# Performance work log

Hardware: AMD Instinct MI355X
Metric: run time of the kernel (lower is better)

Reference implementation:

```python
import jax, jax.numpy as jnp
import numpy as np
import math

B, S, HID = 2, 2048, 2048
NH, NKV, HD = 32, 8, 64
THETA = 10000.0
EPS = 1e-6
LAYER_IDX = 1
LAMBDA_INIT = 0.8 - 0.6 * math.exp(-0.3 * LAYER_IDX)
LAMBDA_STD = 0.1


def setup_inputs() -> dict:
    key = jax.random.key(0)
    ks = jax.random.split(key, 10)
    hidden_states = jax.random.normal(ks[0], (B, S, HID), jnp.float32)
    # RoPE cos/sin, llama convention: emb = cat(freqs, freqs)
    inv_freq = 1.0 / (THETA ** (np.arange(0, HD, 2, dtype=np.float32) / HD))
    freqs = np.outer(np.arange(S, dtype=np.float32), inv_freq)  # [S, HD/2]
    emb = np.concatenate([freqs, freqs], axis=-1)                # [S, HD]
    cos = jnp.broadcast_to(jnp.asarray(np.cos(emb), jnp.float32)[None], (B, S, HD))
    sin = jnp.broadcast_to(jnp.asarray(np.sin(emb), jnp.float32)[None], (B, S, HD))
    # additive causal mask [B,1,S,S]
    causal = jnp.triu(jnp.full((S, S), -1e9, dtype=jnp.float32), k=1)
    attention_mask = jnp.broadcast_to(causal[None, None], (B, 1, S, S))
    sc = 0.02
    wq = sc * jax.random.normal(ks[1], (NH * HD, HID), jnp.float32)
    wk = sc * jax.random.normal(ks[2], (NKV * HD, HID), jnp.float32)
    wv = sc * jax.random.normal(ks[3], (NKV * HD, HID), jnp.float32)
    wo = sc * jax.random.normal(ks[4], (HID, NH * HD), jnp.float32)
    lambda_q1 = LAMBDA_STD * jax.random.normal(ks[5], (HD,), jnp.float32)
    lambda_k1 = LAMBDA_STD * jax.random.normal(ks[6], (HD,), jnp.float32)
    lambda_q2 = LAMBDA_STD * jax.random.normal(ks[7], (HD,), jnp.float32)
    lambda_k2 = LAMBDA_STD * jax.random.normal(ks[8], (HD,), jnp.float32)
    return {"hidden_states": hidden_states, "cos": cos, "sin": sin,
            "attention_mask": attention_mask, "wq": wq, "wk": wk, "wv": wv,
            "wo": wo, "lambda_q1": lambda_q1, "lambda_k1": lambda_k1,
            "lambda_q2": lambda_q2, "lambda_k2": lambda_k2}


def _rotate_half(x):
    x1, x2 = jnp.split(x, 2, axis=-1)
    return jnp.concatenate([-x2, x1], axis=-1)


def reference(hidden_states, cos, sin, attention_mask, wq, wk, wv, wo,
              lambda_q1, lambda_k1, lambda_q2, lambda_k2):
    b, s, _ = hidden_states.shape
    # projections -> [b, h, s, d]
    q = jnp.einsum('bsh,oh->bso', hidden_states, wq).reshape(b, s, NH, HD).transpose(0, 2, 1, 3)
    k = jnp.einsum('bsh,oh->bso', hidden_states, wk).reshape(b, s, NKV, HD).transpose(0, 2, 1, 3)
    v = jnp.einsum('bsh,oh->bso', hidden_states, wv).reshape(b, s, NKV, HD).transpose(0, 2, 1, 3)
    # rotary
    c, sn = cos[:, None], sin[:, None]  # [b,1,s,d]
    q = q * c + _rotate_half(q) * sn
    k = k * c + _rotate_half(k) * sn
    # GQA repeat
    groups = NH // NKV
    k = jnp.repeat(k, groups, axis=1)
    v = jnp.repeat(v, groups, axis=1)
    # diff-attention value trick: pair head i with head i+NH/2 -> [b, NH, s, 2d]
    v = jnp.concatenate([v[:, :NH // 2], v[:, NH // 2:]], axis=-1)  # [b, NH/2, s, 2d]
    v = jnp.concatenate([v, v], axis=1)                              # [b, NH, s, 2d]
    # scores + causal mask, stable softmax in fp32
    aw = jnp.einsum('bhqd,bhkd->bhqk', q, k) / math.sqrt(HD)
    aw = aw + attention_mask
    aw = jax.nn.softmax(aw.astype(jnp.float32), axis=-1).astype(q.dtype)
    ao = jnp.einsum('bhqk,bhkd->bhqd', aw, v)  # [b, NH, s, 2d]
    lam1 = jnp.exp(jnp.sum((lambda_q1 * lambda_k1).astype(jnp.float32)))
    lam2 = jnp.exp(jnp.sum((lambda_q2 * lambda_k2).astype(jnp.float32)))
    lam = (lam1 - lam2).astype(q.dtype) + LAMBDA_INIT
    a1, a2 = ao[:, :NH // 2], ao[:, NH // 2:]
    out = a1 - lam * a2  # [b, NH/2, s, 2d]
    # RMSNorm over last dim (no affine)
    out = out * jax.lax.rsqrt(jnp.mean(out * out, axis=-1, keepdims=True) + EPS)
    out = (1.0 - LAMBDA_INIT) * out
    out = out.transpose(0, 2, 1, 3).reshape(b, s, NH * HD)
    return jnp.einsum('bso,ho->bsh', out, wo)
```

## Files before the change

### kernel.cpp

```cpp
#include <hip/hip_runtime.h>

typedef __attribute__((ext_vector_type(8))) short bhalf8;
typedef __attribute__((ext_vector_type(4))) float floatx4;

constexpr int B_ = 2, S_ = 2048, HID_ = 2048, NH_ = 32, NKV_ = 8, HD_ = 64;
constexpr float LAMBDA_INIT_F = 0.35550906759096924f;
constexpr float EPS_ = 1e-6f;
constexpr float QSCALE_ = 0.18033688011112042f;

#define DEVINL __device__ __forceinline__

DEVINL float bf2f(unsigned short u) {
    union { unsigned u; float f; } v; v.u = ((unsigned)u) << 16; return v.f;
}
DEVINL unsigned short f2bf(float f) {
    union { float f; unsigned u; } v; v.f = f;
    unsigned u = v.u;
    return (unsigned short)((u + 0x7fffu + ((u >> 16) & 1u)) >> 16);
}
DEVINL float fexp2(float x) {
#if __has_builtin(__builtin_amdgcn_exp2f)
    return __builtin_amdgcn_exp2f(x);
#else
    return exp2f(x);
#endif
}
DEVINL unsigned pk_bf16(float a, float b) {
#if __has_builtin(__builtin_amdgcn_cvt_pk_bf16_f32)
    typedef __bf16 bf16x2_t __attribute__((ext_vector_type(2)));
    bf16x2_t p = __builtin_amdgcn_cvt_pk_bf16_f32(a, b);
    unsigned r;
    __builtin_memcpy(&r, &p, 4);
    return r;
#else
    return (unsigned)f2bf(a) | ((unsigned)f2bf(b) << 16);
#endif
}
DEVINL void load_lds16(const unsigned short* g, unsigned short* l) {
    __builtin_amdgcn_global_load_lds(
        (const __attribute__((address_space(1))) unsigned int*)g,
        (__attribute__((address_space(3))) unsigned int*)l, 16, 0, 0);
}

__global__ void cvt_f32_bf16(const float* __restrict__ src, unsigned short* __restrict__ dst, int n) {
    int i = (blockIdx.x * 256 + threadIdx.x) * 4;
    if (i < n) {
        float4 v = *(const float4*)(src + i);
        ushort4 o;
        o.x = f2bf(v.x); o.y = f2bf(v.y); o.z = f2bf(v.z); o.w = f2bf(v.w);
        *(ushort4*)(dst + i) = o;
    }
}

__global__ void lam_kernel(const float* __restrict__ q1, const float* __restrict__ k1,
                           const float* __restrict__ q2, const float* __restrict__ k2,
                           float* __restrict__ lam) {
    const int l = threadIdx.x;
    float p1 = q1[l] * k1[l];
    float p2 = q2[l] * k2[l];
    #pragma unroll
    for (int off = 1; off < 64; off <<= 1) {
        p1 += __shfl_xor(p1, off, 64);
        p2 += __shfl_xor(p2, off, 64);
    }
    if (l == 0) *lam = expf(p1) - expf(p2) + LAMBDA_INIT_F;
}

template <bool OUT_BF16>
__global__ __launch_bounds__(256)
void gemm_bt(const unsigned short* __restrict__ A, const unsigned short* __restrict__ Bw,
             void* __restrict__ Cout, int M, int N, int K) {
    __shared__ __align__(16) unsigned short As[128][32];
    __shared__ __align__(16) unsigned short Bs[128][32];
    const int t = threadIdx.x;
    const int w = t >> 6, lane = t & 63, quad = lane >> 4, lid = lane & 15;
    const int wr = (w >> 1) * 64, wc = (w & 1) * 64;
    const long bm = (long)blockIdx.x * 128, bn = (long)blockIdx.y * 128;

    floatx4 acc[4][4];
    #pragma unroll
    for (int i = 0; i < 4; i++)
        #pragma unroll
        for (int j = 0; j < 4; j++) acc[i][j] = (floatx4){0.f, 0.f, 0.f, 0.f};

    const int s0 = t, s1 = t + 256;
    const unsigned short* Ag0 = A + (bm + (s0 >> 2)) * (long)K + (s0 & 3) * 8;
    const unsigned short* Ag1 = A + (bm + (s1 >> 2)) * (long)K + (s1 & 3) * 8;
    const unsigned short* Bg0 = Bw + (bn + (s0 >> 2)) * (long)K + (s0 & 3) * 8;
    const unsigned short* Bg1 = Bw + (bn + (s1 >> 2)) * (long)K + (s1 & 3) * 8;
    unsigned short* Al0 = &As[0][0] + s0 * 8;
    unsigned short* Al1 = &As[0][0] + s1 * 8;
    unsigned short* Bl0 = &Bs[0][0] + s0 * 8;
    unsigned short* Bl1 = &Bs[0][0] + s1 * 8;

    for (int kt = 0; kt < K; kt += 32) {
        __syncthreads();
        load_lds16(Ag0 + kt, Al0);
        load_lds16(Ag1 + kt, Al1);
        load_lds16(Bg0 + kt, Bl0);
        load_lds16(Bg1 + kt, Bl1);
        __syncthreads();
        bhalf8 af[4], bf[4];
        #pragma unroll
        for (int i = 0; i < 4; i++) af[i] = *(const bhalf8*)&As[wr + i * 16 + lid][quad * 8];
        #pragma unroll
        for (int j = 0; j < 4; j++) bf[j] = *(const bhalf8*)&Bs[wc + j * 16 + lid][quad * 8];
        #pragma unroll
        for (int i = 0; i < 4; i++)
            #pragma unroll
            for (int j = 0; j < 4; j++)
                acc[i][j] = __builtin_amdgcn_mfma_f32_16x16x32_bf16(af[i], bf[j], acc[i][j], 0, 0, 0);
    }

    #pragma unroll
    for (int i = 0; i < 4; i++) {
        #pragma unroll
        for (int j = 0; j < 4; j++) {
            const long row = bm + wr + i * 16 + quad * 4;
            const long col = bn + wc + j * 16 + lid;
            #pragma unroll
            for (int r = 0; r < 4; r++) {
                float v = acc[i][j][r];
                if (OUT_BF16)
                    ((unsigned short*)Cout)[(row + r) * N + col] = f2bf(v);
                else
                    ((float*)Cout)[(row + r) * N + col] = v;
            }
        }
    }
}

__global__ __launch_bounds__(256)
void rope_split(const unsigned short* __restrict__ qkv, const float* __restrict__ cosb,
                const float* __restrict__ sinb, unsigned short* __restrict__ Qr,
                unsigned short* __restrict__ Kr) {
    const int r = blockIdx.x;
    const int b = r >> 11, s = r & 2047;
    const int t = threadIdx.x;
    const unsigned short* rowp = qkv + (size_t)r * 3072;
    #pragma unroll
    for (int i = 0; i < 8; i++) {
        const int c = t * 8 + i;
        const int h = c >> 6, d = c & 63;
        const float x = bf2f(rowp[c]);
        const float oth = bf2f(rowp[(h << 6) + ((d < 32) ? d + 32 : d - 32)]);
        const float rot = (d < 32) ? -oth : oth;
        const float y = x * cosb[(size_t)r * 64 + d] + rot * sinb[(size_t)r * 64 + d];
        Qr[((size_t)(b * NH_ + h) * S_ + s) * HD_ + d] = f2bf(y * QSCALE_);
    }
    #pragma unroll
    for (int i = 0; i < 2; i++) {
        const int c = t * 2 + i;
        const int h = c >> 6, d = c & 63;
        const float x = bf2f(rowp[2048 + c]);
        const float oth = bf2f(rowp[2048 + (h << 6) + ((d < 32) ? d + 32 : d - 32)]);
        const float rot = (d < 32) ? -oth : oth;
        const float y = x * cosb[(size_t)r * 64 + d] + rot * sinb[(size_t)r * 64 + d];
        Kr[((size_t)(b * NKV_ + h) * S_ + s) * HD_ + d] = f2bf(y);
    }
}

__global__ __launch_bounds__(256)
void transpose_v(const unsigned short* __restrict__ qkv, unsigned short* __restrict__ VT) {
    __shared__ __align__(16) unsigned short tile[64][72];
    const int bh = blockIdx.y;
    const int b = bh >> 3, h = bh & 7;
    const int s0 = blockIdx.x * 64;
    const int t = threadIdx.x;
    {
        const int sl = t >> 2, d0 = (t & 3) * 16;
        const unsigned short* src = qkv + (size_t)(b * 2048 + s0 + sl) * 3072 + 2560 + h * 64 + d0;
        *(int4*)&tile[sl][d0] = *(const int4*)src;
        *(int4*)&tile[sl][d0 + 8] = *(const int4*)(src + 8);
    }
    __syncthreads();
    {
        const int dl = t >> 2, sc0 = (t & 3) * 16;
        unsigned short* dst = VT + ((size_t)bh * 64 + dl) * 2048 + s0 + sc0;
        unsigned short out[16];
        #pragma unroll
        for (int i = 0; i < 16; i++) out[i] = tile[sc0 + i][dl];
        *(int4*)dst = *(const int4*)&out[0];
        *(int4*)(dst + 8) = *(const int4*)&out[8];
    }
}

__global__ __launch_bounds__(256)
void attn_diff(const unsigned short* __restrict__ Qr, const unsigned short* __restrict__ Kr,
               const unsigned short* __restrict__ VT, const float* __restrict__ lamp,
               unsigned short* __restrict__ attn) {
    union SM {
        struct {
            unsigned short Kt[2][64][72];
            unsigned short Vt[128][72];
        } a;
        unsigned short Ot[2][32][136];
    };
    __shared__ __align__(16) SM sm;
    unsigned short(*Pt)[16][72] = (unsigned short(*)[16][72]) & sm.a.Kt[0][0][0];

    const int j = blockIdx.y, b = blockIdx.z;
    const int t = threadIdx.x;
    const int w = t >> 6, lane = t & 63, quad = lane >> 4, lid = lane & 15;
    const int st = w >> 1;
    const int rh = (w & 1) * 16;
    const int kv1 = j >> 2, kv2 = 4 + (j >> 2);
    const int qhead = j + st * 16;
    const float lam = *lamp;

    const int ss = t >> 7, key_s = (t & 127) >> 1, dh = (t & 1) * 32;
    const unsigned short* ksrc0 = Kr + (size_t)(b * NKV_ + (ss ? kv2 : kv1)) * S_ * HD_ +
                                  (size_t)key_s * HD_ + dh;
    const int d7 = t >> 1, vh = (t & 1) * 32;
    const unsigned short* vsrc0 = VT + ((size_t)(b * NKV_ + (d7 < 64 ? kv1 : kv2)) * HD_ +
                                        (d7 & 63)) * (size_t)S_ + vh;

    for (int half = 0; half < 2; half++) {
        const int qt = half ? (63 - (int)blockIdx.x) : (int)blockIdx.x;
        const int qb = qt * 32;

        const unsigned short* qbase =
            Qr + ((size_t)((b * NH_ + qhead) * S_) + qb + rh + lid) * HD_;
        const bhalf8 qa0 = *(const bhalf8*)(qbase + quad * 8);
        const bhalf8 qa1 = *(const bhalf8*)(qbase + 32 + quad * 8);

        floatx4 acc[8];
        #pragma unroll
        for (int c = 0; c < 8; c++) acc[c] = (floatx4){0.f, 0.f, 0.f, 0.f};
        float l_acc[4] = {0.f, 0.f, 0.f, 0.f};

        const int row_max_wave = qb + rh + 15;
        const int nkt = ((qb + 31) >> 6) + 1;

        for (int kt = 0; kt < nkt; kt++) {
            const int k0 = kt * 64;
            const unsigned short* kp = ksrc0 + (size_t)k0 * HD_;
            const unsigned short* vp = vsrc0 + k0;
            int4 kr0 = *(const int4*)(kp);
            int4 kr1 = *(const int4*)(kp + 8);
            int4 kr2 = *(const int4*)(kp + 16);
            int4 kr3 = *(const int4*)(kp + 24);
            int4 vr0 = *(const int4*)(vp);
            int4 vr1 = *(const int4*)(vp + 8);
            int4 vr2 = *(const int4*)(vp + 16);
            int4 vr3 = *(const int4*)(vp + 24);
            __syncthreads();
            *(int4*)&sm.a.Kt[ss][key_s][dh] = kr0;
            *(int4*)&sm.a.Kt[ss][key_s][dh + 8] = kr1;
            *(int4*)&sm.a.Kt[ss][key_s][dh + 16] = kr2;
            *(int4*)&sm.a.Kt[ss][key_s][dh + 24] = kr3;
            *(int4*)&sm.a.Vt[d7][vh] = vr0;
            *(int4*)&sm.a.Vt[d7][vh + 8] = vr1;
            *(int4*)&sm.a.Vt[d7][vh + 16] = vr2;
            *(int4*)&sm.a.Vt[d7][vh + 24] = vr3;
            __syncthreads();

            const bool last = (kt == nkt - 1);
            const int nt_lim = last ? (((row_max_wave - k0) >> 4) + 1) : 4;

            floatx4 sc[4];
            #pragma unroll
            for (int nt = 0; nt < 4; nt++) {
                if (nt < nt_lim) {
                    const bhalf8 kb0 = *(const bhalf8*)&sm.a.Kt[st][nt * 16 + lid][quad * 8];
                    const bhalf8 kb1 = *(const bhalf8*)&sm.a.Kt[st][nt * 16 + lid][32 + quad * 8];
                    floatx4 z = (floatx4){0.f, 0.f, 0.f, 0.f};
                    z = __builtin_amdgcn_mfma_f32_16x16x32_bf16(qa0, kb0, z, 0, 0, 0);
                    z = __builtin_amdgcn_mfma_f32_16x16x32_bf16(qa1, kb1, z, 0, 0, 0);
                    sc[nt] = z;
                }
            }

            if (last) {
                #pragma unroll
                for (int nt = 0; nt < 4; nt++) {
                    const int keyg = k0 + nt * 16 + lid;
                    #pragma unroll
                    for (int r = 0; r < 4; r++) {
                        float p = 0.f;
                        if (nt < nt_lim) {
                            const int rowg = qb + rh + quad * 4 + r;
                            p = (keyg > rowg) ? 0.f : fexp2(sc[nt][r]);
                        }
                        sc[nt][r] = p;
                        l_acc[r] += p;
                    }
                }
            } else {
                #pragma unroll
                for (int nt = 0; nt < 4; nt++)
                    #pragma unroll
                    for (int r = 0; r < 4; r++) {
                        const float p = fexp2(sc[nt][r]);
                        sc[nt][r] = p;
                        l_acc[r] += p;
                    }
            }

            __syncthreads();

            #pragma unroll
            for (int nt = 0; nt < 4; nt++) {
                #pragma unroll
                for (int r = 0; r < 4; r += 2) {
                    const unsigned pk = pk_bf16(sc[nt][r], sc[nt][r + 1]);
                    Pt[w][quad * 4 + r][nt * 16 + lid] = (unsigned short)(pk & 0xffff);
                    Pt[w][quad * 4 + r + 1][nt * 16 + lid] = (unsigned short)(pk >> 16);
                }
            }

            #pragma unroll
            for (int kk = 0; kk < 2; kk++) {
                if (nt_lim > kk * 2) {
                    const bhalf8 pa = *(const bhalf8*)&Pt[w][lid][kk * 32 + quad * 8];
                    #pragma unroll
                    for (int c = 0; c < 8; c++) {
                        const bhalf8 vb = *(const bhalf8*)&sm.a.Vt[c * 16 + lid][kk * 32 + quad * 8];
                        acc[c] = __builtin_amdgcn_mfma_f32_16x16x32_bf16(pa, vb, acc[c], 0, 0, 0);
                    }
                }
            }
        }

        #pragma unroll
        for (int off = 1; off < 16; off <<= 1)
            #pragma unroll
            for (int r = 0; r < 4; r++) l_acc[r] += __shfl_xor(l_acc[r], off, 64);

        __syncthreads();
        #pragma unroll
        for (int r = 0; r < 4; r++) {
            const float rl = 1.0f / l_acc[r];
            #pragma unroll
            for (int c = 0; c < 8; c++)
                sm.Ot[st][rh + quad * 4 + r][c * 16 + lid] = f2bf(acc[c][r] * rl);
        }
        __syncthreads();

        const int row = t >> 3, m = t & 7;
        float vals[16];
        float ssum = 0.f;
        #pragma unroll
        for (int c = 0; c < 4; c++) {
            const unsigned long long u0 = *(const unsigned long long*)&sm.Ot[0][row][m * 4 + 32 * c];
            const unsigned long long u1 = *(const unsigned long long*)&sm.Ot[1][row][m * 4 + 32 * c];
            #pragma unroll
            for (int i = 0; i < 4; i++) {
                const float x = bf2f((unsigned short)(u0 >> (16 * i))) -
                                lam * bf2f((unsigned short)(u1 >> (16 * i)));
                vals[c * 4 + i] = x;
                ssum += x * x;
            }
        }
        ssum += __shfl_xor(ssum, 1, 64);
        ssum += __shfl_xor(ssum, 2, 64);
        ssum += __shfl_xor(ssum, 4, 64);
        const float scale = (1.f - LAMBDA_INIT_F) * rsqrtf(ssum * (1.f / 128.f) + EPS_);
        unsigned short* dst = attn + (size_t)(b * S_ + qb + row) * (NH_ * HD_) + j * 128 + m * 4;
        #pragma unroll
        for (int c = 0; c < 4; c++) {
            unsigned short ob[4];
            #pragma unroll
            for (int i = 0; i < 4; i++) ob[i] = f2bf(vals[c * 4 + i] * scale);
            *(unsigned long long*)(dst + 32 * c) = *(const unsigned long long*)ob;
        }
        __syncthreads();
    }
}

extern "C" void kernel_launch(void* const* d_in, const int* in_sizes, int n_in,
                              void* d_out, int out_size, void* d_ws, size_t ws_size,
                              hipStream_t stream) {
    const float* hs   = (const float*)d_in[0];
    const float* cosb = (const float*)d_in[1];
    const float* sinb = (const float*)d_in[2];
    const float* wq   = (const float*)d_in[4];
    const float* wk   = (const float*)d_in[5];
    const float* wv   = (const float*)d_in[6];
    const float* wo   = (const float*)d_in[7];
    const float* lq1  = (const float*)d_in[8];
    const float* lk1  = (const float*)d_in[9];
    const float* lq2  = (const float*)d_in[10];
    const float* lk2  = (const float*)d_in[11];

    unsigned short* p = (unsigned short*)d_ws;
    unsigned short* hs_bf = p;  p += (size_t)4096 * 2048;
    unsigned short* wcat  = p;  p += (size_t)3072 * 2048;
    unsigned short* wo_bf = p;  p += (size_t)2048 * 2048;
    unsigned short* qkv   = p;  p += (size_t)4096 * 3072;
    unsigned short* Qr    = p;  p += (size_t)B_ * NH_ * S_ * HD_;
    unsigned short* Kr    = p;  p += (size_t)B_ * NKV_ * S_ * HD_;
    unsigned short* VT    = p;  p += (size_t)B_ * NKV_ * S_ * HD_;
    unsigned short* attnb = p;  p += (size_t)4096 * 2048;
    float* lam = (float*)p;

    cvt_f32_bf16<<<(4096 * 2048) / 1024, 256, 0, stream>>>(hs, hs_bf, 4096 * 2048);
    cvt_f32_bf16<<<(2048 * 2048) / 1024, 256, 0, stream>>>(wq, wcat, 2048 * 2048);
    cvt_f32_bf16<<<(512 * 2048) / 1024, 256, 0, stream>>>(wk, wcat + (size_t)2048 * 2048, 512 * 2048);
    cvt_f32_bf16<<<(512 * 2048) / 1024, 256, 0, stream>>>(wv, wcat + (size_t)2560 * 2048, 512 * 2048);
    cvt_f32_bf16<<<(2048 * 2048) / 1024, 256, 0, stream>>>(wo, wo_bf, 2048 * 2048);
    lam_kernel<<<1, 64, 0, stream>>>(lq1, lk1, lq2, lk2, lam);

    gemm_bt<true><<<dim3(32, 24), 256, 0, stream>>>(hs_bf, wcat, qkv, 4096, 3072, 2048);
    rope_split<<<4096, 256, 0, stream>>>(qkv, cosb, sinb, Qr, Kr);
    transpose_v<<<dim3(32, 16), 256, 0, stream>>>(qkv, VT);
    attn_diff<<<dim3(32, 16, 2), 256, 0, stream>>>(Qr, Kr, VT, lam, attnb);
    gemm_bt<false><<<dim3(32, 16), 256, 0, stream>>>(attnb, wo_bf, d_out, 4096, 2048, 2048);
}
```

Measured before the change: 426.5 us.

## Double-buffer GEMM LDS, vectorize RoPE, and widen attention tiles to 64 rows

The GEMM now double-buffers its LDS tiles so the next K-slice is loaded while MFMAs run on the current one, leaving one barrier per iteration. RoPE split now uses 16-byte vector loads and stores instead of scalar per-element accesses. The attention kernel moves to 512 threads with 64-row query tiles, giving each wave its own P buffer and removing one barrier. The larger attention block improves K/V reuse per load but raises LDS and register use and may lower occupancy.

```diff
diff --git a/kernel.cpp b/kernel.cpp
--- a/kernel.cpp
+++ b/kernel.cpp
@@ -70,8 +70,8 @@
 __global__ __launch_bounds__(256)
 void gemm_bt(const unsigned short* __restrict__ A, const unsigned short* __restrict__ Bw,
              void* __restrict__ Cout, int M, int N, int K) {
-    __shared__ __align__(16) unsigned short As[128][32];
-    __shared__ __align__(16) unsigned short Bs[128][32];
+    __shared__ __align__(16) unsigned short As[2][128][32];
+    __shared__ __align__(16) unsigned short Bs[2][128][32];
     const int t = threadIdx.x;
     const int w = t >> 6, lane = t & 63, quad = lane >> 4, lid = lane & 15;
     const int wr = (w >> 1) * 64, wc = (w & 1) * 64;
@@ -88,28 +88,35 @@
     const unsigned short* Ag1 = A + (bm + (s1 >> 2)) * (long)K + (s1 & 3) * 8;
     const unsigned short* Bg0 = Bw + (bn + (s0 >> 2)) * (long)K + (s0 & 3) * 8;
     const unsigned short* Bg1 = Bw + (bn + (s1 >> 2)) * (long)K + (s1 & 3) * 8;
-    unsigned short* Al0 = &As[0][0] + s0 * 8;
-    unsigned short* Al1 = &As[0][0] + s1 * 8;
-    unsigned short* Bl0 = &Bs[0][0] + s0 * 8;
-    unsigned short* Bl1 = &Bs[0][0] + s1 * 8;
-
-    for (int kt = 0; kt < K; kt += 32) {
-        __syncthreads();
-        load_lds16(Ag0 + kt, Al0);
-        load_lds16(Ag1 + kt, Al1);
-        load_lds16(Bg0 + kt, Bl0);
-        load_lds16(Bg1 + kt, Bl1);
-        __syncthreads();
+    const int l0 = s0 * 8, l1 = s1 * 8;
+
+    load_lds16(Ag0, &As[0][0][0] + l0);
+    load_lds16(Ag1, &As[0][0][0] + l1);
+    load_lds16(Bg0, &Bs[0][0][0] + l0);
+    load_lds16(Bg1, &Bs[0][0][0] + l1);
+    __syncthreads();
+
+    const int nk = K >> 5;
+    for (int kt = 0; kt < nk; kt++) {
+        const int cur = kt & 1, nxt = cur ^ 1;
+        if (kt + 1 < nk) {
+            const int off = (kt + 1) << 5;
+            load_lds16(Ag0 + off, &As[nxt][0][0] + l0);
+            load_lds16(Ag1 + off, &As[nxt][0][0] + l1);
+            load_lds16(Bg0 + off, &Bs[nxt][0][0] + l0);
+            load_lds16(Bg1 + off, &Bs[nxt][0][0] + l1);
+        }
         bhalf8 af[4], bf[4];
         #pragma unroll
-        for (int i = 0; i < 4; i++) af[i] = *(const bhalf8*)&As[wr + i * 16 + lid][quad * 8];
-        #pragma unroll
-        for (int j = 0; j < 4; j++) bf[j] = *(const bhalf8*)&Bs[wc + j * 16 + lid][quad * 8];
+        for (int i = 0; i < 4; i++) af[i] = *(const bhalf8*)&As[cur][wr + i * 16 + lid][quad * 8];
+        #pragma unroll
+        for (int j = 0; j < 4; j++) bf[j] = *(const bhalf8*)&Bs[cur][wc + j * 16 + lid][quad * 8];
         #pragma unroll
         for (int i = 0; i < 4; i++)
             #pragma unroll
             for (int j = 0; j < 4; j++)
                 acc[i][j] = __builtin_amdgcn_mfma_f32_16x16x32_bf16(af[i], bf[j], acc[i][j], 0, 0, 0);
+        __syncthreads();
     }
 
     #pragma unroll
@@ -138,25 +145,41 @@
     const int b = r >> 11, s = r & 2047;
     const int t = threadIdx.x;
     const unsigned short* rowp = qkv + (size_t)r * 3072;
-    #pragma unroll
-    for (int i = 0; i < 8; i++) {
-        const int c = t * 8 + i;
-        const int h = c >> 6, d = c & 63;
-        const float x = bf2f(rowp[c]);
-        const float oth = bf2f(rowp[(h << 6) + ((d < 32) ? d + 32 : d - 32)]);
-        const float rot = (d < 32) ? -oth : oth;
-        const float y = x * cosb[(size_t)r * 64 + d] + rot * sinb[(size_t)r * 64 + d];
-        Qr[((size_t)(b * NH_ + h) * S_ + s) * HD_ + d] = f2bf(y * QSCALE_);
-    }
-    #pragma unroll
-    for (int i = 0; i < 2; i++) {
-        const int c = t * 2 + i;
-        const int h = c >> 6, d = c & 63;
-        const float x = bf2f(rowp[2048 + c]);
-        const float oth = bf2f(rowp[2048 + (h << 6) + ((d < 32) ? d + 32 : d - 32)]);
-        const float rot = (d < 32) ? -oth : oth;
-        const float y = x * cosb[(size_t)r * 64 + d] + rot * sinb[(size_t)r * 64 + d];
-        Kr[((size_t)(b * NKV_ + h) * S_ + s) * HD_ + d] = f2bf(y);
+    const float* cp = cosb + (size_t)r * 64;
+    const float* sp = sinb + (size_t)r * 64;
+    {
+        const int h = t >> 3, d0 = (t & 7) * 8;
+        unsigned short x[8], o[8], y[8];
+        *(int4*)x = *(const int4*)(rowp + h * 64 + d0);
+        const int od = (d0 < 32) ? d0 + 32 : d0 - 32;
+        *(int4*)o = *(const int4*)(rowp + h * 64 + od);
+        const float sgn = (d0 < 32) ? -1.f : 1.f;
+        float cc[8], sn[8];
+        *(float4*)&cc[0] = *(const float4*)(cp + d0);
+        *(float4*)&cc[4] = *(const float4*)(cp + d0 + 4);
+        *(float4*)&sn[0] = *(const float4*)(sp + d0);
+        *(float4*)&sn[4] = *(const float4*)(sp + d0 + 4);
+        #pragma unroll
+        for (int i = 0; i < 8; i++)
+            y[i] = f2bf((bf2f(x[i]) * cc[i] + sgn * bf2f(o[i]) * sn[i]) * QSCALE_);
+        *(int4*)(Qr + ((size_t)(b * NH_ + h) * S_ + s) * HD_ + d0) = *(const int4*)y;
+    }
+    if (t < 64) {
+        const int h = t >> 3, d0 = (t & 7) * 8;
+        unsigned short x[8], o[8], y[8];
+        *(int4*)x = *(const int4*)(rowp + 2048 + h * 64 + d0);
+        const int od = (d0 < 32) ? d0 + 32 : d0 - 32;
+        *(int4*)o = *(const int4*)(rowp + 2048 + h * 64 + od);
+        const float sgn = (d0 < 32) ? -1.f : 1.f;
+        float cc[8], sn[8];
+        *(float4*)&cc[0] = *(const float4*)(cp + d0);
+        *(float4*)&cc[4] = *(const float4*)(cp + d0 + 4);
+        *(float4*)&sn[0] = *(const float4*)(sp + d0);
+        *(float4*)&sn[4] = *(const float4*)(sp + d0 + 4);
+        #pragma unroll
+        for (int i = 0; i < 8; i++)
+            y[i] = f2bf(bf2f(x[i]) * cc[i] + sgn * bf2f(o[i]) * sn[i]);
+        *(int4*)(Kr + ((size_t)(b * NKV_ + h) * S_ + s) * HD_ + d0) = *(const int4*)y;
     }
 }
 
@@ -185,7 +208,7 @@
     }
 }
 
-__global__ __launch_bounds__(256)
+__global__ __launch_bounds__(512, 4)
 void attn_diff(const unsigned short* __restrict__ Qr, const unsigned short* __restrict__ Kr,
                const unsigned short* __restrict__ VT, const float* __restrict__ lamp,
                unsigned short* __restrict__ attn) {
@@ -193,31 +216,32 @@
         struct {
             unsigned short Kt[2][64][72];
             unsigned short Vt[128][72];
+            unsigned short Pt[8][16][72];
         } a;
-        unsigned short Ot[2][32][136];
+        unsigned short Ot[2][64][136];
     };
     __shared__ __align__(16) SM sm;
-    unsigned short(*Pt)[16][72] = (unsigned short(*)[16][72]) & sm.a.Kt[0][0][0];
 
     const int j = blockIdx.y, b = blockIdx.z;
     const int t = threadIdx.x;
     const int w = t >> 6, lane = t & 63, quad = lane >> 4, lid = lane & 15;
-    const int st = w >> 1;
-    const int rh = (w & 1) * 16;
+    const int st = w >> 2;
+    const int rh = (w & 3) * 16;
     const int kv1 = j >> 2, kv2 = 4 + (j >> 2);
     const int qhead = j + st * 16;
     const float lam = *lamp;
 
-    const int ss = t >> 7, key_s = (t & 127) >> 1, dh = (t & 1) * 32;
+    const int ss = t >> 8, kidx = t & 255;
+    const int key_s = kidx >> 2, dh = (kidx & 3) * 16;
     const unsigned short* ksrc0 = Kr + (size_t)(b * NKV_ + (ss ? kv2 : kv1)) * S_ * HD_ +
                                   (size_t)key_s * HD_ + dh;
-    const int d7 = t >> 1, vh = (t & 1) * 32;
+    const int d7 = t >> 2, vh = (t & 3) * 16;
     const unsigned short* vsrc0 = VT + ((size_t)(b * NKV_ + (d7 < 64 ? kv1 : kv2)) * HD_ +
                                         (d7 & 63)) * (size_t)S_ + vh;
 
     for (int half = 0; half < 2; half++) {
-        const int qt = half ? (63 - (int)blockIdx.x) : (int)blockIdx.x;
-        const int qb = qt * 32;
+        const int qt = half ? (31 - (int)blockIdx.x) : (int)blockIdx.x;
+        const int qb = qt * 64;
 
         const unsigned short* qbase =
             Qr + ((size_t)((b * NH_ + qhead) * S_) + qb + rh + lid) * HD_;
@@ -229,8 +253,7 @@
         for (int c = 0; c < 8; c++) acc[c] = (floatx4){0.f, 0.f, 0.f, 0.f};
         float l_acc[4] = {0.f, 0.f, 0.f, 0.f};
 
-        const int row_max_wave = qb + rh + 15;
-        const int nkt = ((qb + 31) >> 6) + 1;
+        const int nkt = qt + 1;
 
         for (int kt = 0; kt < nkt; kt++) {
             const int k0 = kt * 64;
@@ -238,25 +261,17 @@
             const unsigned short* vp = vsrc0 + k0;
             int4 kr0 = *(const int4*)(kp);
             int4 kr1 = *(const int4*)(kp + 8);
-            int4 kr2 = *(const int4*)(kp + 16);
-            int4 kr3 = *(const int4*)(kp + 24);
             int4 vr0 = *(const int4*)(vp);
             int4 vr1 = *(const int4*)(vp + 8);
-            int4 vr2 = *(const int4*)(vp + 16);
-            int4 vr3 = *(const int4*)(vp + 24);
             __syncthreads();
             *(int4*)&sm.a.Kt[ss][key_s][dh] = kr0;
             *(int4*)&sm.a.Kt[ss][key_s][dh + 8] = kr1;
-            *(int4*)&sm.a.Kt[ss][key_s][dh + 16] = kr2;
-            *(int4*)&sm.a.Kt[ss][key_s][dh + 24] = kr3;
             *(int4*)&sm.a.Vt[d7][vh] = vr0;
             *(int4*)&sm.a.Vt[d7][vh + 8] = vr1;
-            *(int4*)&sm.a.Vt[d7][vh + 16] = vr2;
-            *(int4*)&sm.a.Vt[d7][vh + 24] = vr3;
             __syncthreads();
 
             const bool last = (kt == nkt - 1);
-            const int nt_lim = last ? (((row_max_wave - k0) >> 4) + 1) : 4;
+            const int nt_lim = last ? ((w & 3) + 1) : 4;
 
             floatx4 sc[4];
             #pragma unroll
@@ -297,22 +312,20 @@
                     }
             }
 
-            __syncthreads();
-
             #pragma unroll
             for (int nt = 0; nt < 4; nt++) {
                 #pragma unroll
                 for (int r = 0; r < 4; r += 2) {
                     const unsigned pk = pk_bf16(sc[nt][r], sc[nt][r + 1]);
-                    Pt[w][quad * 4 + r][nt * 16 + lid] = (unsigned short)(pk & 0xffff);
-                    Pt[w][quad * 4 + r + 1][nt * 16 + lid] = (unsigned short)(pk >> 16);
+                    sm.a.Pt[w][quad * 4 + r][nt * 16 + lid] = (unsigned short)(pk & 0xffff);
+                    sm.a.Pt[w][quad * 4 + r + 1][nt * 16 + lid] = (unsigned short)(pk >> 16);
                 }
             }
 
             #pragma unroll
             for (int kk = 0; kk < 2; kk++) {
                 if (nt_lim > kk * 2) {
-                    const bhalf8 pa = *(const bhalf8*)&Pt[w][lid][kk * 32 + quad * 8];
+                    const bhalf8 pa = *(const bhalf8*)&sm.a.Pt[w][lid][kk * 32 + quad * 8];
                     #pragma unroll
                     for (int c = 0; c < 8; c++) {
                         const bhalf8 vb = *(const bhalf8*)&sm.a.Vt[c * 16 + lid][kk * 32 + quad * 8];
@@ -404,6 +417,6 @@
     gemm_bt<true><<<dim3(32, 24), 256, 0, stream>>>(hs_bf, wcat, qkv, 4096, 3072, 2048);
     rope_split<<<4096, 256, 0, stream>>>(qkv, cosb, sinb, Qr, Kr);
     transpose_v<<<dim3(32, 16), 256, 0, stream>>>(qkv, VT);
-    attn_diff<<<dim3(32, 16, 2), 256, 0, stream>>>(Qr, Kr, VT, lam, attnb);
+    attn_diff<<<dim3(16, 16, 2), 512, 0, stream>>>(Qr, Kr, VT, lam, attnb);
     gemm_bt<false><<<dim3(32, 16), 256, 0, stream>>>(attnb, wo_bf, d_out, 4096, 2048, 2048);
 }
```

Measured after the change: 365.4 us. -14.3%, faster.
